# Kernel tuning notes

Measured on AMD Instinct MI355X. Metric: run time of the kernel, lower is better.

## Reference

```python
import jax, jax.numpy as jnp
import numpy as np

D, H, DH = 64, 4, 32
INNER = H * DH
SCALE = 1.0 / np.sqrt(DH)


def _layernorm(x, w, b, eps=1e-5):
    mu = jnp.mean(x, axis=-1, keepdims=True)
    var = jnp.var(x, axis=-1, keepdims=True)
    return (x - mu) * jax.lax.rsqrt(var + eps) * w + b


def setup_inputs() -> dict:
    key = jax.random.key(0)
    ks = jax.random.split(key, 8)
    B, N = 1, 256
    z = jax.random.normal(ks[0], (B, N, N, D), dtype=jnp.float32)
    mask = jax.random.randint(ks[1], (B, N, N), 0, 2).astype(jnp.bool_)
    ln_w = jnp.ones((D,), jnp.float32)
    ln_b = jnp.zeros((D,), jnp.float32)
    w_qkv = jax.random.normal(ks[2], (3 * INNER, D), jnp.float32) * 0.02
    w_bias = jax.random.normal(ks[3], (H, D), jnp.float32) * 0.02
    w_out = jax.random.normal(ks[4], (D, INNER), jnp.float32) * 0.02
    w_gate = jax.random.normal(ks[5], (INNER, D), jnp.float32) * 0.02
    return {"z": z, "mask": mask, "ln_w": ln_w, "ln_b": ln_b,
            "w_qkv": w_qkv, "w_bias": w_bias, "w_out": w_out, "w_gate": w_gate}


def reference(z, mask, ln_w, ln_b, w_qkv, w_bias, w_out, w_gate):
    # mode == 'starting': attend along the second pair axis per row n.
    B, N = z.shape[0], z.shape[1]
    h = _layernorm(z, ln_w, ln_b)                       # [B,N,N,D]
    qkv = jnp.einsum('bijd,ed->bije', h, w_qkv)         # [B,N,N,3*INNER]
    qkv = qkv.reshape(B, N, N, 3, H, DH)
    q, k, v = qkv[..., 0, :, :], qkv[..., 1, :, :], qkv[..., 2, :, :]  # [B,N,N,H,dh]
    attn = jnp.einsum('bnihd,bnjhd->bnhij', q, k) * SCALE  # [B,N,H,N,N]
    bias = jnp.einsum('bijd,hd->bhij', h, w_bias)          # [B,H,N,N]
    attn = attn + bias[:, None]                            # broadcast over n
    big_neg = jnp.finfo(attn.dtype).min
    attn = jnp.where(mask[:, :, None, None, :], attn, big_neg)  # mask keys j per (b,n)
    attn = jax.nn.softmax(attn, axis=-1)
    out = jnp.einsum('bnhij,bnjhd->bnihd', attn, v)        # [B,N,N,H,dh]
    out = out.reshape(B, N, N, INNER)
    gate = jax.nn.sigmoid(jnp.einsum('bijd,ed->bije', h, w_gate))
    out = jnp.einsum('bije,de->bijd', out * gate, w_out)
    return out
```

## Files before the change

### kernel.cpp

```cpp
#include <hip/hip_runtime.h>
#include <hip/hip_bf16.h>

#define N_ 256
#define D_ 64
#define H_ 4
#define DH_ 32
#define EQKV 384
#define NPOS 65536
#define SCALE_F 0.17677669529663687f
#define BIG_NEG -3.402823466e38f
#define P_STRIDE 264
#define H_STRIDE 72
#define X_STRIDE 136
#define A_STRIDE 136
#define O_STRIDE 68
#define Q_STRIDE 392

typedef __attribute__((ext_vector_type(8))) short s16x8;
typedef __attribute__((ext_vector_type(4))) float f32x4;


__device__ inline short bfbits(float x) {
    __hip_bfloat16 b = __float2bfloat16(x);
    return *reinterpret_cast<short*>(&b);
}
__device__ inline float b2f(short s) {
    unsigned u = ((unsigned)(unsigned short)s) << 16;
    union { unsigned u; float f; } c; c.u = u; return c.f;
}
__device__ inline s16x8 cvt8(float4 a, float4 b) {
    s16x8 r;
    r[0] = bfbits(a.x); r[1] = bfbits(a.y); r[2] = bfbits(a.z); r[3] = bfbits(a.w);
    r[4] = bfbits(b.x); r[5] = bfbits(b.y); r[6] = bfbits(b.z); r[7] = bfbits(b.w);
    return r;
}

__global__ __launch_bounds__(512) void k1_ln_proj_mfma(
    const float* __restrict__ z, const float* __restrict__ ln_w, const float* __restrict__ ln_b,
    const float* __restrict__ w_qkv, const float* __restrict__ w_bias,
    __hip_bfloat16* __restrict__ qkv_ws, __hip_bfloat16* __restrict__ h_ws,
    float* __restrict__ bias_ws)
{
    __shared__ __align__(16) short smem[64 * Q_STRIDE];
    const int t = threadIdx.x;
    const int wave = t >> 6, lane = t & 63;
    const int pos0 = blockIdx.x * 64;
    const int m = lane & 15, quad = lane >> 4;

    {
        const float lw = ln_w[lane], lb = ln_b[lane];
        const float wb0 = w_bias[lane], wb1 = w_bias[64 + lane],
                    wb2 = w_bias[128 + lane], wb3 = w_bias[192 + lane];
        for (int pp = 0; pp < 8; ++pp) {
            const int p = wave * 8 + pp;
            const float zv = z[(size_t)(pos0 + p) * 64 + lane];
            float s = zv, s2 = zv * zv;
            #pragma unroll
            for (int off = 32; off; off >>= 1) { s += __shfl_xor(s, off); s2 += __shfl_xor(s2, off); }
            const float mu = s * 0.015625f;
            const float var = s2 * 0.015625f - mu * mu;
            const float rs = rsqrtf(var + 1e-5f);
            const float hv = (zv - mu) * rs * lw + lb;
            smem[p * H_STRIDE + lane] = bfbits(hv);
            float b0 = hv * wb0, b1 = hv * wb1, b2 = hv * wb2, b3 = hv * wb3;
            #pragma unroll
            for (int off = 32; off; off >>= 1) {
                b0 += __shfl_xor(b0, off); b1 += __shfl_xor(b1, off);
                b2 += __shfl_xor(b2, off); b3 += __shfl_xor(b3, off);
            }
            if (lane < 4) {
                const int gpos = pos0 + p;
                const int gi = gpos >> 8, gj = gpos & 255;
                const float bv = lane == 0 ? b0 : lane == 1 ? b1 : lane == 2 ? b2 : b3;
                bias_ws[lane * NPOS + gi * 256 + gj] = bv;
            }
        }
    }
    __syncthreads();

    {
        const int row = t >> 3, c8 = (t & 7) * 8;
        *(s16x8*)(h_ws + (size_t)(pos0 + row) * 64 + c8) =
            *(const s16x8*)(smem + row * H_STRIDE + c8);
    }

    const int colbase = wave * 48;
    s16x8 bfrag[3][2];
    #pragma unroll
    for (int nt = 0; nt < 3; ++nt) {
        const int col = colbase + nt * 16 + m;
        const float* wp = w_qkv + (size_t)col * 64;
        #pragma unroll
        for (int kt = 0; kt < 2; ++kt) {
            const float4 w0 = *(const float4*)(wp + kt * 32 + quad * 8);
            const float4 w1 = *(const float4*)(wp + kt * 32 + quad * 8 + 4);
            bfrag[nt][kt] = cvt8(w0, w1);
        }
    }

    s16x8 afrag[4][2];
    #pragma unroll
    for (int mt = 0; mt < 4; ++mt)
        #pragma unroll
        for (int kt = 0; kt < 2; ++kt)
            afrag[mt][kt] = *(const s16x8*)(smem + (mt * 16 + m) * H_STRIDE + kt * 32 + quad * 8);

    f32x4 acc[4][3];
    #pragma unroll
    for (int mt = 0; mt < 4; ++mt)
        #pragma unroll
        for (int nt = 0; nt < 3; ++nt)
            acc[mt][nt] = (f32x4){0.f, 0.f, 0.f, 0.f};

    #pragma unroll
    for (int kt = 0; kt < 2; ++kt)
        #pragma unroll
        for (int mt = 0; mt < 4; ++mt)
            #pragma unroll
            for (int nt = 0; nt < 3; ++nt)
                acc[mt][nt] = __builtin_amdgcn_mfma_f32_16x16x32_bf16(
                    afrag[mt][kt], bfrag[nt][kt], acc[mt][nt], 0, 0, 0);

    __syncthreads();

    #pragma unroll
    for (int mt = 0; mt < 4; ++mt)
        #pragma unroll
        for (int nt = 0; nt < 3; ++nt) {
            const int c = colbase + nt * 16 + m;
            #pragma unroll
            for (int r = 0; r < 4; ++r) {
                const int row = mt * 16 + quad * 4 + r;
                smem[row * Q_STRIDE + c] = bfbits(acc[mt][nt][r]);
            }
        }
    __syncthreads();

    #pragma unroll
    for (int i = 0; i < 6; ++i) {
        const int idx = i * 512 + t;
        const int row = idx / 48, c8 = (idx % 48) * 8;
        *(s16x8*)(qkv_ws + (size_t)(pos0 + row) * EQKV + c8) =
            *(const s16x8*)(smem + row * Q_STRIDE + c8);
    }
}

__global__ __launch_bounds__(512, 4) void k2_attn_mfma(
    const __hip_bfloat16* __restrict__ qkv_ws, const float* __restrict__ bias_ws,
    const int* __restrict__ mask, __hip_bfloat16* __restrict__ attn_bf)
{
    __shared__ __align__(16) short p_s[64 * P_STRIDE];
    __shared__ __align__(16) short vt_s[32 * P_STRIDE];
    __shared__ float keep[256];
    __shared__ float redl[64][2];

    const int bx = blockIdx.x;
    const int n = bx & 255, h = bx >> 8;
    const int t = threadIdx.x;
    const int wave = t >> 6, lane = t & 63;
    const int m = lane & 15, quad = lane >> 4;
    const int mt = wave & 3, nh = wave >> 2;

    if (t < 256) keep[t] = (mask[n * 256 + t] != 0) ? 1.0f : 0.0f;

    {
        const int j = t >> 1, dh = (t & 1) * 16;
        const __hip_bfloat16* vp = qkv_ws + (size_t)(n * 256 + j) * 384 + 256 + h * 32 + dh;
        s16x8 v0 = *(const s16x8*)vp;
        s16x8 v1 = *(const s16x8*)(vp + 8);
        #pragma unroll
        for (int e = 0; e < 8; ++e) {
            vt_s[(dh + e) * P_STRIDE + j]     = v0[e];
            vt_s[(dh + 8 + e) * P_STRIDE + j] = v1[e];
        }
    }

    s16x8 kf[8];
    #pragma unroll
    for (int tt = 0; tt < 8; ++tt) {
        const int jt = nh * 8 + tt;
        kf[tt] = *(const s16x8*)(qkv_ws + (size_t)(n * 256 + jt * 16 + m) * 384 + 128 + h * 32 + quad * 8);
    }

    const int jcol0 = nh * 128 + m;
    const float* bias_h = bias_ws + (size_t)h * NPOS;
    s16x8 qf = *(const s16x8*)(qkv_ws + (size_t)(n * 256 + mt * 16 + m) * 384 + h * 32 + quad * 8);
    float bb[8][4];
    #pragma unroll
    for (int tt = 0; tt < 8; ++tt)
        #pragma unroll
        for (int r = 0; r < 4; ++r)
            bb[tt][r] = bias_h[(mt * 16 + quad * 4 + r) * 256 + jcol0 + tt * 16];

    __syncthreads();

    for (int ig = 0; ig < 4; ++ig) {
        const int i0 = ig * 64;

        f32x4 s[8];
        #pragma unroll
        for (int tt = 0; tt < 8; ++tt) {
            f32x4 z4 = {0.f, 0.f, 0.f, 0.f};
            s[tt] = __builtin_amdgcn_mfma_f32_16x16x32_bf16(qf, kf[tt], z4, 0, 0, 0);
        }
        #pragma unroll
        for (int tt = 0; tt < 8; ++tt) {
            const float kp = keep[jcol0 + tt * 16];
            #pragma unroll
            for (int r = 0; r < 4; ++r) {
                const float sv = s[tt][r] * SCALE_F + bb[tt][r];
                s[tt][r] = (kp != 0.f) ? sv : BIG_NEG;
            }
        }

        {
            float ls[4];
            #pragma unroll
            for (int r = 0; r < 4; ++r) {
                float acc = 0.f;
                #pragma unroll
                for (int tt = 0; tt < 8; ++tt) {
                    const float p = __expf(s[tt][r]);
                    s[tt][r] = p;
                    acc += p;
                }
                #pragma unroll
                for (int off = 1; off < 16; off <<= 1) acc += __shfl_xor(acc, off);
                ls[r] = acc;
            }
            if (m == 0) {
                #pragma unroll
                for (int r = 0; r < 4; ++r) redl[mt * 16 + quad * 4 + r][nh] = ls[r];
            }
            #pragma unroll
            for (int tt = 0; tt < 8; ++tt) {
                const int col = (nh * 8 + tt) * 16 + m;
                #pragma unroll
                for (int r = 0; r < 4; ++r) {
                    const int row = mt * 16 + quad * 4 + r;
                    p_s[row * P_STRIDE + col] = bfbits(s[tt][r]);
                }
            }
        }

        if (ig < 3) {
            const int i0n = i0 + 64;
            qf = *(const s16x8*)(qkv_ws + (size_t)(n * 256 + i0n + mt * 16 + m) * 384 + h * 32 + quad * 8);
            #pragma unroll
            for (int tt = 0; tt < 8; ++tt)
                #pragma unroll
                for (int r = 0; r < 4; ++r)
                    bb[tt][r] = bias_h[(i0n + mt * 16 + quad * 4 + r) * 256 + jcol0 + tt * 16];
        }
        __syncthreads();

        {
            f32x4 o0 = {0.f, 0.f, 0.f, 0.f};
            f32x4 o1 = {0.f, 0.f, 0.f, 0.f};
            const int arow = mt * 16 + m;
            const int brow = nh * 16 + m;
            #pragma unroll
            for (int kt = 0; kt < 4; ++kt) {
                const s16x8 ap0 = *(const s16x8*)(p_s + arow * P_STRIDE + (2 * kt) * 32 + quad * 8);
                const s16x8 bv0 = *(const s16x8*)(vt_s + brow * P_STRIDE + (2 * kt) * 32 + quad * 8);
                o0 = __builtin_amdgcn_mfma_f32_16x16x32_bf16(ap0, bv0, o0, 0, 0, 0);
                const s16x8 ap1 = *(const s16x8*)(p_s + arow * P_STRIDE + (2 * kt + 1) * 32 + quad * 8);
                const s16x8 bv1 = *(const s16x8*)(vt_s + brow * P_STRIDE + (2 * kt + 1) * 32 + quad * 8);
                o1 = __builtin_amdgcn_mfma_f32_16x16x32_bf16(ap1, bv1, o1, 0, 0, 0);
            }
            #pragma unroll
            for (int r = 0; r < 4; ++r) {
                const int row = mt * 16 + quad * 4 + r;
                const float l = fmaxf(redl[row][0] + redl[row][1], 1e-30f);
                const float val = (o0[r] + o1[r]) * (1.0f / l);
                const int ig_row = i0 + row;
                attn_bf[(size_t)(n * 256 + ig_row) * 128 + h * 32 + nh * 16 + m] = __float2bfloat16(val);
            }
        }
        __syncthreads();
    }
}

__global__ __launch_bounds__(512) void k3_proj_mfma(
    const __hip_bfloat16* __restrict__ attn_bf, const __hip_bfloat16* __restrict__ h_ws,
    const float* __restrict__ w_gate, const float* __restrict__ w_out, float* __restrict__ out)
{
    __shared__ __align__(16) short h_s[64 * H_STRIDE];
    __shared__ __align__(16) short a_s[64 * A_STRIDE];
    __shared__ __align__(16) short x_s[64 * X_STRIDE];
    const int t = threadIdx.x;
    const int wave = t >> 6, lane = t & 63;
    const int pos0 = blockIdx.x * 64;
    const int m = lane & 15, quad = lane >> 4;

    {
        const int row = t >> 3, c8 = (t & 7) * 8;
        *(s16x8*)(h_s + row * H_STRIDE + c8) =
            *(const s16x8*)(h_ws + (size_t)(pos0 + row) * 64 + c8);
    }
    #pragma unroll
    for (int i = 0; i < 2; ++i) {
        const int idx = i * 512 + t;
        const int row = idx >> 4, c8 = (idx & 15) * 8;
        *(s16x8*)(a_s + row * A_STRIDE + c8) =
            *(const s16x8*)(attn_bf + (size_t)(pos0 + row) * 128 + c8);
    }
    __syncthreads();

    {
        const int mt = wave & 3, cg = wave >> 2;
        s16x8 ha[2];
        #pragma unroll
        for (int kt = 0; kt < 2; ++kt)
            ha[kt] = *(const s16x8*)(h_s + (mt * 16 + m) * H_STRIDE + kt * 32 + quad * 8);
        #pragma unroll
        for (int nt = 0; nt < 4; ++nt) {
            const float* wp = w_gate + (size_t)(cg * 64 + nt * 16 + m) * 64;
            const s16x8 b0 = cvt8(*(const float4*)(wp + quad * 8),
                                  *(const float4*)(wp + quad * 8 + 4));
            const s16x8 b1 = cvt8(*(const float4*)(wp + 32 + quad * 8),
                                  *(const float4*)(wp + 32 + quad * 8 + 4));
            f32x4 g4 = (f32x4){0.f, 0.f, 0.f, 0.f};
            g4 = __builtin_amdgcn_mfma_f32_16x16x32_bf16(ha[0], b0, g4, 0, 0, 0);
            g4 = __builtin_amdgcn_mfma_f32_16x16x32_bf16(ha[1], b1, g4, 0, 0, 0);
            const int col = cg * 64 + nt * 16 + m;
            #pragma unroll
            for (int r = 0; r < 4; ++r) {
                const int row = mt * 16 + quad * 4 + r;
                const float gv = 1.0f / (1.0f + __expf(-g4[r]));
                x_s[row * X_STRIDE + col] = bfbits(b2f(a_s[row * A_STRIDE + col]) * gv);
            }
        }
    }
    __syncthreads();

    const int mt = wave & 3, nh = wave >> 2;
    s16x8 bfrag[2][4];
    #pragma unroll
    for (int nt = 0; nt < 2; ++nt) {
        const int d = nh * 32 + nt * 16 + m;
        const float* wp = w_out + (size_t)d * 128;
        #pragma unroll
        for (int kt = 0; kt < 4; ++kt) {
            const float4 w0 = *(const float4*)(wp + kt * 32 + quad * 8);
            const float4 w1 = *(const float4*)(wp + kt * 32 + quad * 8 + 4);
            bfrag[nt][kt] = cvt8(w0, w1);
        }
    }

    s16x8 afrag[4];
    #pragma unroll
    for (int kt = 0; kt < 4; ++kt)
        afrag[kt] = *(const s16x8*)(x_s + (mt * 16 + m) * X_STRIDE + kt * 32 + quad * 8);

    f32x4 acc[2];
    acc[0] = (f32x4){0.f, 0.f, 0.f, 0.f};
    acc[1] = (f32x4){0.f, 0.f, 0.f, 0.f};
    #pragma unroll
    for (int kt = 0; kt < 4; ++kt) {
        acc[0] = __builtin_amdgcn_mfma_f32_16x16x32_bf16(afrag[kt], bfrag[0][kt], acc[0], 0, 0, 0);
        acc[1] = __builtin_amdgcn_mfma_f32_16x16x32_bf16(afrag[kt], bfrag[1][kt], acc[1], 0, 0, 0);
    }

    float* o_s = (float*)a_s;
    #pragma unroll
    for (int nt = 0; nt < 2; ++nt) {
        const int d = nh * 32 + nt * 16 + m;
        #pragma unroll
        for (int r = 0; r < 4; ++r) {
            const int row = mt * 16 + quad * 4 + r;
            o_s[row * O_STRIDE + d] = acc[nt][r];
        }
    }
    __syncthreads();

    #pragma unroll
    for (int i = 0; i < 2; ++i) {
        const int idx = i * 512 + t;
        const int row = idx >> 4, c4 = (idx & 15) * 4;
        *(float4*)(out + (size_t)(pos0 + row) * 64 + c4) =
            *(const float4*)(o_s + row * O_STRIDE + c4);
    }
}

extern "C" void kernel_launch(void* const* d_in, const int* in_sizes, int n_in,
                              void* d_out, int out_size, void* d_ws, size_t ws_size,
                              hipStream_t stream) {
    const float* z      = (const float*)d_in[0];
    const int*   mask   = (const int*)d_in[1];
    const float* ln_w   = (const float*)d_in[2];
    const float* ln_b   = (const float*)d_in[3];
    const float* w_qkv  = (const float*)d_in[4];
    const float* w_bias = (const float*)d_in[5];
    const float* w_out  = (const float*)d_in[6];
    const float* w_gate = (const float*)d_in[7];
    float* out = (float*)d_out;

    char* ws = (char*)d_ws;
    __hip_bfloat16* qkv_ws  = (__hip_bfloat16*)(ws);
    float*          bias_ws = (float*)(ws + 50331648);
    __hip_bfloat16* h_ws    = (__hip_bfloat16*)(ws + 51380224);
    __hip_bfloat16* attn_bf = (__hip_bfloat16*)(ws + 59768832);

    k1_ln_proj_mfma<<<1024, 512, 0, stream>>>(z, ln_w, ln_b, w_qkv, w_bias,
                                              qkv_ws, h_ws, bias_ws);
    k2_attn_mfma<<<1024, 512, 0, stream>>>(qkv_ws, bias_ws, mask, attn_bf);
    k3_proj_mfma<<<1024, 512, 0, stream>>>(attn_bf, h_ws, w_gate, w_out, out);
}
```

Measured before the change: 197.4 us.

## Fuse attention and gated output projection into one per-row kernel

Merges the attention kernel and the gate/output projection kernel into one kernel. Each 1024-thread block processes one row n over all heads and keeps the attention output in shared memory. This removes the global write and read of the intermediate attention tensor and one kernel launch. The cost is a large shared-memory footprint, one block per CU, and heads processed serially inside each block, which lowers occupancy and latency hiding.

```diff
diff --git a/kernel.cpp b/kernel.cpp
--- a/kernel.cpp
+++ b/kernel.cpp
@@ -9,12 +9,11 @@
 #define NPOS 65536
 #define SCALE_F 0.17677669529663687f
 #define BIG_NEG -3.402823466e38f
-#define P_STRIDE 264
 #define H_STRIDE 72
-#define X_STRIDE 136
-#define A_STRIDE 136
-#define O_STRIDE 68
 #define Q_STRIDE 392
+#define PS 264
+#define OXS 136
+#define OFS 68
 
 typedef __attribute__((ext_vector_type(8))) short s16x8;
 typedef __attribute__((ext_vector_type(4))) float f32x4;
@@ -145,76 +144,70 @@
     }
 }
 
-__global__ __launch_bounds__(512, 4) void k2_attn_mfma(
+__global__ __launch_bounds__(1024, 4) void k2_fused(
     const __hip_bfloat16* __restrict__ qkv_ws, const float* __restrict__ bias_ws,
-    const int* __restrict__ mask, __hip_bfloat16* __restrict__ attn_bf)
+    const int* __restrict__ mask, const __hip_bfloat16* __restrict__ h_ws,
+    const float* __restrict__ w_gate, const float* __restrict__ w_out,
+    float* __restrict__ out)
 {
-    __shared__ __align__(16) short p_s[64 * P_STRIDE];
-    __shared__ __align__(16) short vt_s[32 * P_STRIDE];
-    __shared__ float keep[256];
-    __shared__ float redl[64][2];
-
-    const int bx = blockIdx.x;
-    const int n = bx & 255, h = bx >> 8;
+    __shared__ __align__(16) char smem_raw[156160];
+    short* o_x  = (short*)smem_raw;
+    short* p_s  = (short*)(smem_raw + 69632);
+    short* vt_s = (short*)(smem_raw + 137216);
+    float* keep = (float*)(smem_raw + 154112);
+    float* redl = (float*)(smem_raw + 155136);
+
+    const int n = blockIdx.x;
     const int t = threadIdx.x;
     const int wave = t >> 6, lane = t & 63;
     const int m = lane & 15, quad = lane >> 4;
-    const int mt = wave & 3, nh = wave >> 2;
+    const int mt = wave & 7;
+    const int nh = wave >> 3;
+    const int jcol0 = nh * 128 + m;
 
     if (t < 256) keep[t] = (mask[n * 256 + t] != 0) ? 1.0f : 0.0f;
-
-    {
-        const int j = t >> 1, dh = (t & 1) * 16;
-        const __hip_bfloat16* vp = qkv_ws + (size_t)(n * 256 + j) * 384 + 256 + h * 32 + dh;
-        s16x8 v0 = *(const s16x8*)vp;
-        s16x8 v1 = *(const s16x8*)(vp + 8);
-        #pragma unroll
-        for (int e = 0; e < 8; ++e) {
-            vt_s[(dh + e) * P_STRIDE + j]     = v0[e];
-            vt_s[(dh + 8 + e) * P_STRIDE + j] = v1[e];
-        }
-    }
-
-    s16x8 kf[8];
-    #pragma unroll
-    for (int tt = 0; tt < 8; ++tt) {
-        const int jt = nh * 8 + tt;
-        kf[tt] = *(const s16x8*)(qkv_ws + (size_t)(n * 256 + jt * 16 + m) * 384 + 128 + h * 32 + quad * 8);
-    }
-
-    const int jcol0 = nh * 128 + m;
-    const float* bias_h = bias_ws + (size_t)h * NPOS;
-    s16x8 qf = *(const s16x8*)(qkv_ws + (size_t)(n * 256 + mt * 16 + m) * 384 + h * 32 + quad * 8);
-    float bb[8][4];
-    #pragma unroll
-    for (int tt = 0; tt < 8; ++tt)
-        #pragma unroll
-        for (int r = 0; r < 4; ++r)
-            bb[tt][r] = bias_h[(mt * 16 + quad * 4 + r) * 256 + jcol0 + tt * 16];
-
-    __syncthreads();
-
-    for (int ig = 0; ig < 4; ++ig) {
-        const int i0 = ig * 64;
-
-        f32x4 s[8];
-        #pragma unroll
-        for (int tt = 0; tt < 8; ++tt) {
-            f32x4 z4 = {0.f, 0.f, 0.f, 0.f};
-            s[tt] = __builtin_amdgcn_mfma_f32_16x16x32_bf16(qf, kf[tt], z4, 0, 0, 0);
-        }
-        #pragma unroll
-        for (int tt = 0; tt < 8; ++tt) {
-            const float kp = keep[jcol0 + tt * 16];
-            #pragma unroll
-            for (int r = 0; r < 4; ++r) {
-                const float sv = s[tt][r] * SCALE_F + bb[tt][r];
-                s[tt][r] = (kp != 0.f) ? sv : BIG_NEG;
-            }
-        }
-
+    __syncthreads();
+
+    for (int h = 0; h < 4; ++h) {
         {
-            float ls[4];
+            const int j = t >> 2, dh0 = (t & 3) * 8;
+            const s16x8 v = *(const s16x8*)(qkv_ws + (size_t)(n * 256 + j) * 384 + 256 + h * 32 + dh0);
+            #pragma unroll
+            for (int e = 0; e < 8; ++e) vt_s[(dh0 + e) * PS + j] = v[e];
+        }
+        s16x8 kf[8];
+        #pragma unroll
+        for (int tt = 0; tt < 8; ++tt)
+            kf[tt] = *(const s16x8*)(qkv_ws + (size_t)(n * 256 + (nh * 8 + tt) * 16 + m) * 384 + 128 + h * 32 + quad * 8);
+        const float* bias_h = bias_ws + (size_t)h * NPOS;
+        s16x8 qf = *(const s16x8*)(qkv_ws + (size_t)(n * 256 + mt * 16 + m) * 384 + h * 32 + quad * 8);
+
+        for (int ig = 0; ig < 2; ++ig) {
+            const int i0 = ig * 128;
+
+            float bb[8][4];
+            #pragma unroll
+            for (int tt = 0; tt < 8; ++tt)
+                #pragma unroll
+                for (int r = 0; r < 4; ++r)
+                    bb[tt][r] = bias_h[(i0 + mt * 16 + quad * 4 + r) * 256 + jcol0 + tt * 16];
+
+            f32x4 s[8];
+            #pragma unroll
+            for (int tt = 0; tt < 8; ++tt) {
+                f32x4 z4 = {0.f, 0.f, 0.f, 0.f};
+                s[tt] = __builtin_amdgcn_mfma_f32_16x16x32_bf16(qf, kf[tt], z4, 0, 0, 0);
+            }
+            #pragma unroll
+            for (int tt = 0; tt < 8; ++tt) {
+                const float kp = keep[jcol0 + tt * 16];
+                #pragma unroll
+                for (int r = 0; r < 4; ++r) {
+                    const float sv = s[tt][r] * SCALE_F + bb[tt][r];
+                    s[tt][r] = (kp != 0.f) ? sv : BIG_NEG;
+                }
+            }
+
             #pragma unroll
             for (int r = 0; r < 4; ++r) {
                 float acc = 0.f;
@@ -226,96 +219,69 @@
                 }
                 #pragma unroll
                 for (int off = 1; off < 16; off <<= 1) acc += __shfl_xor(acc, off);
-                ls[r] = acc;
-            }
-            if (m == 0) {
-                #pragma unroll
-                for (int r = 0; r < 4; ++r) redl[mt * 16 + quad * 4 + r][nh] = ls[r];
+                if (m == 0) redl[(mt * 16 + quad * 4 + r) * 2 + nh] = acc;
             }
             #pragma unroll
             for (int tt = 0; tt < 8; ++tt) {
-                const int col = (nh * 8 + tt) * 16 + m;
+                const int col = jcol0 + tt * 16;
+                #pragma unroll
+                for (int r = 0; r < 4; ++r)
+                    p_s[(mt * 16 + quad * 4 + r) * PS + col] = bfbits(s[tt][r]);
+            }
+
+            if (!(h == 3 && ig == 1)) {
+                const int hn  = (ig == 0) ? h : h + 1;
+                const int i0n = (ig == 0) ? 128 : 0;
+                qf = *(const s16x8*)(qkv_ws + (size_t)(n * 256 + i0n + mt * 16 + m) * 384 + hn * 32 + quad * 8);
+            }
+            __syncthreads();
+
+            {
+                const int dt = nh;
+                f32x4 o0 = {0.f, 0.f, 0.f, 0.f};
+                f32x4 o1 = {0.f, 0.f, 0.f, 0.f};
+                const int arow = mt * 16 + m;
+                const int brow = dt * 16 + m;
+                #pragma unroll
+                for (int kt = 0; kt < 4; ++kt) {
+                    const s16x8 ap0 = *(const s16x8*)(p_s + arow * PS + (2 * kt) * 32 + quad * 8);
+                    const s16x8 bv0 = *(const s16x8*)(vt_s + brow * PS + (2 * kt) * 32 + quad * 8);
+                    o0 = __builtin_amdgcn_mfma_f32_16x16x32_bf16(ap0, bv0, o0, 0, 0, 0);
+                    const s16x8 ap1 = *(const s16x8*)(p_s + arow * PS + (2 * kt + 1) * 32 + quad * 8);
+                    const s16x8 bv1 = *(const s16x8*)(vt_s + brow * PS + (2 * kt + 1) * 32 + quad * 8);
+                    o1 = __builtin_amdgcn_mfma_f32_16x16x32_bf16(ap1, bv1, o1, 0, 0, 0);
+                }
                 #pragma unroll
                 for (int r = 0; r < 4; ++r) {
                     const int row = mt * 16 + quad * 4 + r;
-                    p_s[row * P_STRIDE + col] = bfbits(s[tt][r]);
+                    const float l = fmaxf(redl[row * 2] + redl[row * 2 + 1], 1e-30f);
+                    o_x[(i0 + row) * OXS + h * 32 + dt * 16 + m] =
+                        bfbits((o0[r] + o1[r]) * (1.0f / l));
                 }
             }
-        }
-
-        if (ig < 3) {
-            const int i0n = i0 + 64;
-            qf = *(const s16x8*)(qkv_ws + (size_t)(n * 256 + i0n + mt * 16 + m) * 384 + h * 32 + quad * 8);
-            #pragma unroll
-            for (int tt = 0; tt < 8; ++tt)
-                #pragma unroll
-                for (int r = 0; r < 4; ++r)
-                    bb[tt][r] = bias_h[(i0n + mt * 16 + quad * 4 + r) * 256 + jcol0 + tt * 16];
-        }
-        __syncthreads();
-
-        {
-            f32x4 o0 = {0.f, 0.f, 0.f, 0.f};
-            f32x4 o1 = {0.f, 0.f, 0.f, 0.f};
-            const int arow = mt * 16 + m;
-            const int brow = nh * 16 + m;
-            #pragma unroll
-            for (int kt = 0; kt < 4; ++kt) {
-                const s16x8 ap0 = *(const s16x8*)(p_s + arow * P_STRIDE + (2 * kt) * 32 + quad * 8);
-                const s16x8 bv0 = *(const s16x8*)(vt_s + brow * P_STRIDE + (2 * kt) * 32 + quad * 8);
-                o0 = __builtin_amdgcn_mfma_f32_16x16x32_bf16(ap0, bv0, o0, 0, 0, 0);
-                const s16x8 ap1 = *(const s16x8*)(p_s + arow * P_STRIDE + (2 * kt + 1) * 32 + quad * 8);
-                const s16x8 bv1 = *(const s16x8*)(vt_s + brow * P_STRIDE + (2 * kt + 1) * 32 + quad * 8);
-                o1 = __builtin_amdgcn_mfma_f32_16x16x32_bf16(ap1, bv1, o1, 0, 0, 0);
-            }
-            #pragma unroll
-            for (int r = 0; r < 4; ++r) {
-                const int row = mt * 16 + quad * 4 + r;
-                const float l = fmaxf(redl[row][0] + redl[row][1], 1e-30f);
-                const float val = (o0[r] + o1[r]) * (1.0f / l);
-                const int ig_row = i0 + row;
-                attn_bf[(size_t)(n * 256 + ig_row) * 128 + h * 32 + nh * 16 + m] = __float2bfloat16(val);
-            }
-        }
-        __syncthreads();
-    }
-}
-
-__global__ __launch_bounds__(512) void k3_proj_mfma(
-    const __hip_bfloat16* __restrict__ attn_bf, const __hip_bfloat16* __restrict__ h_ws,
-    const float* __restrict__ w_gate, const float* __restrict__ w_out, float* __restrict__ out)
-{
-    __shared__ __align__(16) short h_s[64 * H_STRIDE];
-    __shared__ __align__(16) short a_s[64 * A_STRIDE];
-    __shared__ __align__(16) short x_s[64 * X_STRIDE];
-    const int t = threadIdx.x;
-    const int wave = t >> 6, lane = t & 63;
-    const int pos0 = blockIdx.x * 64;
-    const int m = lane & 15, quad = lane >> 4;
-
-    {
-        const int row = t >> 3, c8 = (t & 7) * 8;
+            __syncthreads();
+        }
+    }
+
+    short* h_s = p_s;
+    #pragma unroll
+    for (int i = 0; i < 2; ++i) {
+        const int idx = i * 1024 + t;
+        const int row = idx >> 3, c8 = (idx & 7) * 8;
         *(s16x8*)(h_s + row * H_STRIDE + c8) =
-            *(const s16x8*)(h_ws + (size_t)(pos0 + row) * 64 + c8);
-    }
-    #pragma unroll
-    for (int i = 0; i < 2; ++i) {
-        const int idx = i * 512 + t;
-        const int row = idx >> 4, c8 = (idx & 15) * 8;
-        *(s16x8*)(a_s + row * A_STRIDE + c8) =
-            *(const s16x8*)(attn_bf + (size_t)(pos0 + row) * 128 + c8);
-    }
-    __syncthreads();
-
-    {
-        const int mt = wave & 3, cg = wave >> 2;
+            *(const s16x8*)(h_ws + (size_t)(n * 256 + row) * 64 + c8);
+    }
+    __syncthreads();
+
+    {
+        const int rt = wave;
         s16x8 ha[2];
         #pragma unroll
         for (int kt = 0; kt < 2; ++kt)
-            ha[kt] = *(const s16x8*)(h_s + (mt * 16 + m) * H_STRIDE + kt * 32 + quad * 8);
-        #pragma unroll
-        for (int nt = 0; nt < 4; ++nt) {
-            const float* wp = w_gate + (size_t)(cg * 64 + nt * 16 + m) * 64;
+            ha[kt] = *(const s16x8*)(h_s + (rt * 16 + m) * H_STRIDE + kt * 32 + quad * 8);
+        #pragma unroll
+        for (int ct = 0; ct < 8; ++ct) {
+            const float* wp = w_gate + (size_t)(ct * 16 + m) * 64;
             const s16x8 b0 = cvt8(*(const float4*)(wp + quad * 8),
                                   *(const float4*)(wp + quad * 8 + 4));
             const s16x8 b1 = cvt8(*(const float4*)(wp + 32 + quad * 8),
@@ -323,63 +289,55 @@
             f32x4 g4 = (f32x4){0.f, 0.f, 0.f, 0.f};
             g4 = __builtin_amdgcn_mfma_f32_16x16x32_bf16(ha[0], b0, g4, 0, 0, 0);
             g4 = __builtin_amdgcn_mfma_f32_16x16x32_bf16(ha[1], b1, g4, 0, 0, 0);
-            const int col = cg * 64 + nt * 16 + m;
             #pragma unroll
             for (int r = 0; r < 4; ++r) {
-                const int row = mt * 16 + quad * 4 + r;
+                const int row = rt * 16 + quad * 4 + r;
+                const int col = ct * 16 + m;
                 const float gv = 1.0f / (1.0f + __expf(-g4[r]));
-                x_s[row * X_STRIDE + col] = bfbits(b2f(a_s[row * A_STRIDE + col]) * gv);
-            }
-        }
-    }
-    __syncthreads();
-
-    const int mt = wave & 3, nh = wave >> 2;
-    s16x8 bfrag[2][4];
-    #pragma unroll
-    for (int nt = 0; nt < 2; ++nt) {
-        const int d = nh * 32 + nt * 16 + m;
-        const float* wp = w_out + (size_t)d * 128;
-        #pragma unroll
-        for (int kt = 0; kt < 4; ++kt) {
-            const float4 w0 = *(const float4*)(wp + kt * 32 + quad * 8);
-            const float4 w1 = *(const float4*)(wp + kt * 32 + quad * 8 + 4);
-            bfrag[nt][kt] = cvt8(w0, w1);
-        }
-    }
-
-    s16x8 afrag[4];
-    #pragma unroll
-    for (int kt = 0; kt < 4; ++kt)
-        afrag[kt] = *(const s16x8*)(x_s + (mt * 16 + m) * X_STRIDE + kt * 32 + quad * 8);
-
-    f32x4 acc[2];
-    acc[0] = (f32x4){0.f, 0.f, 0.f, 0.f};
-    acc[1] = (f32x4){0.f, 0.f, 0.f, 0.f};
-    #pragma unroll
-    for (int kt = 0; kt < 4; ++kt) {
-        acc[0] = __builtin_amdgcn_mfma_f32_16x16x32_bf16(afrag[kt], bfrag[0][kt], acc[0], 0, 0, 0);
-        acc[1] = __builtin_amdgcn_mfma_f32_16x16x32_bf16(afrag[kt], bfrag[1][kt], acc[1], 0, 0, 0);
-    }
-
-    float* o_s = (float*)a_s;
-    #pragma unroll
-    for (int nt = 0; nt < 2; ++nt) {
-        const int d = nh * 32 + nt * 16 + m;
-        #pragma unroll
-        for (int r = 0; r < 4; ++r) {
-            const int row = mt * 16 + quad * 4 + r;
-            o_s[row * O_STRIDE + d] = acc[nt][r];
-        }
-    }
-    __syncthreads();
-
-    #pragma unroll
-    for (int i = 0; i < 2; ++i) {
-        const int idx = i * 512 + t;
-        const int row = idx >> 4, c4 = (idx & 15) * 4;
-        *(float4*)(out + (size_t)(pos0 + row) * 64 + c4) =
-            *(const float4*)(o_s + row * O_STRIDE + c4);
+                o_x[row * OXS + col] = bfbits(b2f(o_x[row * OXS + col]) * gv);
+            }
+        }
+    }
+    __syncthreads();
+
+    {
+        const int rt = wave;
+        s16x8 afrag[4];
+        #pragma unroll
+        for (int kt = 0; kt < 4; ++kt)
+            afrag[kt] = *(const s16x8*)(o_x + (rt * 16 + m) * OXS + kt * 32 + quad * 8);
+        f32x4 acc[4];
+        #pragma unroll
+        for (int nt = 0; nt < 4; ++nt) acc[nt] = (f32x4){0.f, 0.f, 0.f, 0.f};
+        #pragma unroll
+        for (int nt = 0; nt < 4; ++nt) {
+            const float* wp = w_out + (size_t)(nt * 16 + m) * 128;
+            #pragma unroll
+            for (int kt = 0; kt < 4; ++kt) {
+                const s16x8 bf = cvt8(*(const float4*)(wp + kt * 32 + quad * 8),
+                                      *(const float4*)(wp + kt * 32 + quad * 8 + 4));
+                acc[nt] = __builtin_amdgcn_mfma_f32_16x16x32_bf16(afrag[kt], bf, acc[nt], 0, 0, 0);
+            }
+        }
+        __syncthreads();
+        float* o_f = (float*)o_x;
+        #pragma unroll
+        for (int nt = 0; nt < 4; ++nt)
+            #pragma unroll
+            for (int r = 0; r < 4; ++r)
+                o_f[(rt * 16 + quad * 4 + r) * OFS + nt * 16 + m] = acc[nt][r];
+    }
+    __syncthreads();
+
+    {
+        const float* o_f = (const float*)o_x;
+        #pragma unroll
+        for (int i = 0; i < 4; ++i) {
+            const int idx = i * 1024 + t;
+            const int row = idx >> 4, c4 = (idx & 15) * 4;
+            *(float4*)(out + (size_t)(n * 256 + row) * 64 + c4) =
+                *(const float4*)(o_f + row * OFS + c4);
+        }
     }
 }
 
@@ -400,10 +358,9 @@
     __hip_bfloat16* qkv_ws  = (__hip_bfloat16*)(ws);
     float*          bias_ws = (float*)(ws + 50331648);
     __hip_bfloat16* h_ws    = (__hip_bfloat16*)(ws + 51380224);
-    __hip_bfloat16* attn_bf = (__hip_bfloat16*)(ws + 59768832);
 
     k1_ln_proj_mfma<<<1024, 512, 0, stream>>>(z, ln_w, ln_b, w_qkv, w_bias,
                                               qkv_ws, h_ws, bias_ws);
-    k2_attn_mfma<<<1024, 512, 0, stream>>>(qkv_ws, bias_ws, mask, attn_bf);
-    k3_proj_mfma<<<1024, 512, 0, stream>>>(attn_bf, h_ws, w_gate, w_out, out);
-}
+    k2_fused<<<256, 1024, 0, stream>>>(qkv_ws, bias_ws, mask, h_ws,
+                                       w_gate, w_out, out);
+}
```

Measured after the change: 257.1 us. +30.2%, slower.
